# Performance work log

Hardware: AMD Instinct MI355X
Metric: run time of the kernel (lower is better)

The kernel has to match this reference:

```python
import jax, jax.numpy as jnp
import numpy as np
import math

B, C, HW = 4, 256, 32          # batch, seq_len (=channels), spatial side
D_MODEL = HW * HW              # 1024
OUT_C = 32 * 32                # 1024
D_STATE = 16
EXPAND = 2
D_INNER = EXPAND * D_MODEL     # 2048
DT_RANK = math.ceil(D_MODEL / 16)  # 64
D_CONV = 4


def setup_inputs() -> dict:
    key = jax.random.key(0)
    ks = jax.random.split(key, 12)
    s = 0.02
    x1 = jax.random.normal(ks[0], (B, C, HW, HW), dtype=jnp.float32)
    in_proj_w = jax.random.normal(ks[1], (2 * D_INNER, D_MODEL), dtype=jnp.float32) * s
    conv_w = jax.random.normal(ks[2], (D_INNER, 1, D_CONV), dtype=jnp.float32) * s
    conv_b = jnp.zeros((D_INNER,), dtype=jnp.float32)
    x_proj_w = jax.random.normal(ks[3], (DT_RANK + 2 * D_STATE, D_INNER), dtype=jnp.float32) * s
    dt_proj_w = jax.random.normal(ks[4], (D_INNER, DT_RANK), dtype=jnp.float32) * s
    dt_proj_b = jnp.zeros((D_INNER,), dtype=jnp.float32)
    A_log = jnp.log(jnp.broadcast_to(jnp.arange(1, D_STATE + 1, dtype=jnp.float32), (D_INNER, D_STATE)))
    D = jnp.ones((D_INNER,), dtype=jnp.float32)
    out_proj_w = jax.random.normal(ks[5], (OUT_C, D_INNER), dtype=jnp.float32) * s
    ln_w = jnp.ones((OUT_C,), dtype=jnp.float32)
    ln_b = jnp.zeros((OUT_C,), dtype=jnp.float32)
    return {"x1": x1, "in_proj_w": in_proj_w, "conv_w": conv_w, "conv_b": conv_b,
            "x_proj_w": x_proj_w, "dt_proj_w": dt_proj_w, "dt_proj_b": dt_proj_b,
            "A_log": A_log, "D": D, "out_proj_w": out_proj_w, "ln_w": ln_w, "ln_b": ln_b}


def _mamba_forward(x, in_proj_w, conv_w, conv_b, x_proj_w, dt_proj_w, dt_proj_b, A_log, D, out_proj_w):
    # x: (B, L, d_model)
    xz = jnp.einsum('bld,ed->ble', x, in_proj_w)            # (B,L,2*d_inner)
    xs, res = jnp.split(xz, 2, axis=-1)                     # each (B,L,d_inner)
    # depthwise causal conv1d, padding=d_conv-1 then truncate to L (== left pad)
    xs_c = jnp.transpose(xs, (0, 2, 1))                     # (B,d_inner,L)
    xs_c = jax.lax.conv_general_dilated(
        xs_c, conv_w, window_strides=(1,), padding=[(D_CONV - 1, 0)],
        dimension_numbers=('NCH', 'OIH', 'NCH'), feature_group_count=D_INNER)
    xs_c = xs_c + conv_b[None, :, None]
    xs = jax.nn.silu(jnp.transpose(xs_c, (0, 2, 1)))        # (B,L,d_inner)
    # input-dependent SSM parameters
    x_dbl = jnp.einsum('bld,ed->ble', xs, x_proj_w)         # (B,L,dt_rank+2N)
    dt, Bm, Cm = jnp.split(x_dbl, [DT_RANK, DT_RANK + D_STATE], axis=-1)
    delta = jax.nn.softplus(jnp.einsum('blr,dr->bld', dt, dt_proj_w) + dt_proj_b)  # (B,L,d_inner)
    A = -jnp.exp(A_log)                                     # (d_inner, N)
    deltaA = jnp.exp(delta[..., None] * A)                  # (B,L,d_inner,N)
    deltaB_u = delta[..., None] * Bm[:, :, None, :] * xs[..., None]  # (B,L,d_inner,N)

    def step(h, inp):
        dA, dBu, Ct = inp                                   # (B,d,N),(B,d,N),(B,N)
        h = dA * h + dBu
        y = jnp.einsum('bdn,bn->bd', h, Ct)
        return h, y

    h0 = jnp.zeros((deltaA.shape[0], D_INNER, D_STATE), dtype=deltaA.dtype)
    _, ys = jax.lax.scan(step, h0, (jnp.transpose(deltaA, (1, 0, 2, 3)),
                                    jnp.transpose(deltaB_u, (1, 0, 2, 3)),
                                    jnp.transpose(Cm, (1, 0, 2))))
    y = jnp.transpose(ys, (1, 0, 2))                        # (B,L,d_inner)
    y = y + D * xs
    y = y * jax.nn.silu(res)
    return jnp.einsum('bld,od->blo', y, out_proj_w)         # (B,L,out_c)


def reference(x1, in_proj_w, conv_w, conv_b, x_proj_w, dt_proj_w, dt_proj_b,
              A_log, D, out_proj_w, ln_w, ln_b):
    b, c, h, w = x1.shape
    x = x1.reshape(b, c, h * w)                             # (B, L=c, d_model)
    y = _mamba_forward(x, in_proj_w, conv_w, conv_b, x_proj_w, dt_proj_w,
                       dt_proj_b, A_log, D, out_proj_w)
    mu = jnp.mean(y, axis=-1, keepdims=True)
    var = jnp.var(y, axis=-1, keepdims=True)
    y = (y - mu) * jax.lax.rsqrt(var + 1e-5) * ln_w + ln_b
    return y.reshape(b, c, 32, 32)
```

## Files before the change

### kernel.cpp

```cpp
#include <hip/hip_runtime.h>
#include <hip/hip_bf16.h>
#include <math.h>

#define BATCH 4
#define SEQL 256
#define DMODEL 1024
#define DINNER 2048
#define DSTATE 16
#define DTRANK 64
#define OUTC 1024
#define NROWS (BATCH * SEQL)

typedef __attribute__((ext_vector_type(8))) short bf16x8;
typedef __attribute__((ext_vector_type(4))) float f32x4;

__global__ __launch_bounds__(256) void gemm_mfma(const __hip_bfloat16* __restrict__ A,
                                                 const __hip_bfloat16* __restrict__ B,
                                                 float* __restrict__ C,
                                                 int M, int N, int K,
                                                 int lda, int ldb) {
    __shared__ __hip_bfloat16 As[128 * 32];
    __shared__ __hip_bfloat16 Bs[128 * 32];
    const int t  = threadIdx.x;
    const int w  = t >> 6;
    const int ln = t & 63;
    const int wm = w >> 1, wn = w & 1;
    const int q  = ln >> 4, lr = ln & 15;
    const int m0 = blockIdx.y * 128;
    const int n0 = blockIdx.x * 128;
    const int Kpart = K / gridDim.z;
    const int kbase = blockIdx.z * Kpart;

    f32x4 acc[4][4] = {};

    const __hip_bfloat16* Ag = A + (size_t)m0 * lda + kbase;
    const __hip_bfloat16* Bg = B + (size_t)n0 * ldb + kbase;

    for (int k0 = 0; k0 < Kpart; k0 += 32) {
        #pragma unroll
        for (int i = 0; i < 2; ++i) {
            const int c = (i * 4 + w) * 64 + ln;
            const int r = c >> 2, col = (c & 3) * 8;
            __builtin_amdgcn_global_load_lds(
                (const __attribute__((address_space(1))) void*)(Ag + (size_t)r * lda + k0 + col),
                (__attribute__((address_space(3))) void*)(As + (i * 4 + w) * 64 * 8),
                16, 0, 0);
            __builtin_amdgcn_global_load_lds(
                (const __attribute__((address_space(1))) void*)(Bg + (size_t)r * ldb + k0 + col),
                (__attribute__((address_space(3))) void*)(Bs + (i * 4 + w) * 64 * 8),
                16, 0, 0);
        }
        __syncthreads();
        bf16x8 af[4], bfr[4];
        #pragma unroll
        for (int i = 0; i < 4; ++i)
            af[i] = *(const bf16x8*)(As + (wm * 64 + i * 16 + lr) * 32 + q * 8);
        #pragma unroll
        for (int j = 0; j < 4; ++j)
            bfr[j] = *(const bf16x8*)(Bs + (wn * 64 + j * 16 + lr) * 32 + q * 8);
        #pragma unroll
        for (int i = 0; i < 4; ++i)
            #pragma unroll
            for (int j = 0; j < 4; ++j)
                acc[i][j] = __builtin_amdgcn_mfma_f32_16x16x32_bf16(af[i], bfr[j], acc[i][j], 0, 0, 0);
        __syncthreads();
    }
    float* Cz = C + (size_t)blockIdx.z * M * N;
    #pragma unroll
    for (int i = 0; i < 4; ++i) {
        const int mrow = m0 + wm * 64 + i * 16 + q * 4;
        #pragma unroll
        for (int j = 0; j < 4; ++j) {
            const int ncol = n0 + wn * 64 + j * 16 + lr;
            #pragma unroll
            for (int r = 0; r < 4; ++r)
                Cz[(size_t)(mrow + r) * N + ncol] = acc[i][j][r];
        }
    }
}

__global__ __launch_bounds__(256) void gemm_dtsp(const __hip_bfloat16* __restrict__ A,
                                                 const __hip_bfloat16* __restrict__ B,
                                                 const float* __restrict__ bd,
                                                 float* __restrict__ delta) {
    __shared__ __hip_bfloat16 As[128 * 32];
    __shared__ __hip_bfloat16 Bs[128 * 32];
    const int t  = threadIdx.x;
    const int w  = t >> 6;
    const int ln = t & 63;
    const int wm = w >> 1, wn = w & 1;
    const int q  = ln >> 4, lr = ln & 15;
    const int m0 = blockIdx.y * 128;
    const int n0 = blockIdx.x * 128;
    const int lda = 128, ldb = 64, N = 2048;

    f32x4 acc[4][4] = {};
    const __hip_bfloat16* Ag = A + (size_t)m0 * lda;
    const __hip_bfloat16* Bg = B + (size_t)n0 * ldb;

    for (int k0 = 0; k0 < 64; k0 += 32) {
        #pragma unroll
        for (int i = 0; i < 2; ++i) {
            const int c = (i * 4 + w) * 64 + ln;
            const int r = c >> 2, col = (c & 3) * 8;
            __builtin_amdgcn_global_load_lds(
                (const __attribute__((address_space(1))) void*)(Ag + (size_t)r * lda + k0 + col),
                (__attribute__((address_space(3))) void*)(As + (i * 4 + w) * 64 * 8),
                16, 0, 0);
            __builtin_amdgcn_global_load_lds(
                (const __attribute__((address_space(1))) void*)(Bg + (size_t)r * ldb + k0 + col),
                (__attribute__((address_space(3))) void*)(Bs + (i * 4 + w) * 64 * 8),
                16, 0, 0);
        }
        __syncthreads();
        bf16x8 af[4], bfr[4];
        #pragma unroll
        for (int i = 0; i < 4; ++i)
            af[i] = *(const bf16x8*)(As + (wm * 64 + i * 16 + lr) * 32 + q * 8);
        #pragma unroll
        for (int j = 0; j < 4; ++j)
            bfr[j] = *(const bf16x8*)(Bs + (wn * 64 + j * 16 + lr) * 32 + q * 8);
        #pragma unroll
        for (int i = 0; i < 4; ++i)
            #pragma unroll
            for (int j = 0; j < 4; ++j)
                acc[i][j] = __builtin_amdgcn_mfma_f32_16x16x32_bf16(af[i], bfr[j], acc[i][j], 0, 0, 0);
        __syncthreads();
    }
    #pragma unroll
    for (int i = 0; i < 4; ++i) {
        const int mrow = m0 + wm * 64 + i * 16 + q * 4;
        #pragma unroll
        for (int j = 0; j < 4; ++j) {
            const int ncol = n0 + wn * 64 + j * 16 + lr;
            const float bias = bd[ncol];
            #pragma unroll
            for (int r = 0; r < 4; ++r) {
                float v = acc[i][j][r] + bias;
                float sp = (v > 20.f) ? v : log1pf(__expf(v));
                delta[(size_t)(mrow + r) * N + ncol] = sp;
            }
        }
    }
}

__global__ void xdbl_reduce_kernel(const float* __restrict__ part,
                                   float* __restrict__ xdbl,
                                   __hip_bfloat16* __restrict__ xdblb) {
    const int i = blockIdx.x * 256 + threadIdx.x;
    float s = 0.f;
    #pragma unroll
    for (int z = 0; z < 8; ++z) s += part[(size_t)z * (1024 * 128) + i];
    xdbl[i] = s;
    xdblb[i] = __float2bfloat16(s);
}

#define R0 (1024 * 1024)
#define R1 (R0 + 4096 * 1024)
#define R2 (R1 + 2048 * 1024)
#define R3 (R2 + 128 * 2048)
#define R4 (R3 + 2048 * 64)
__global__ void cast_all_kernel(const float* __restrict__ x1,
                                const float* __restrict__ w_in,
                                const float* __restrict__ w_out,
                                const float* __restrict__ w_xp,
                                const float* __restrict__ w_dt,
                                __hip_bfloat16* __restrict__ xa,
                                __hip_bfloat16* __restrict__ wb1,
                                __hip_bfloat16* __restrict__ wob,
                                __hip_bfloat16* __restrict__ wpb,
                                __hip_bfloat16* __restrict__ wdb) {
    int i = blockIdx.x * 256 + threadIdx.x;
    if (i < R0) {
        xa[i] = __float2bfloat16(x1[i]);
    } else if (i < R1) {
        int j = i - R0; wb1[j] = __float2bfloat16(w_in[j]);
    } else if (i < R2) {
        int j = i - R1; wob[j] = __float2bfloat16(w_out[j]);
    } else if (i < R3) {
        int j = i - R2; int e = j >> 11;
        wpb[j] = __float2bfloat16(e < 96 ? w_xp[j] : 0.f);
    } else if (i < R4) {
        int j = i - R3; wdb[j] = __float2bfloat16(w_dt[j]);
    }
}

__global__ void conv_silu_kernel(const float* __restrict__ xz,
                                 const float* __restrict__ conv_w,
                                 const float* __restrict__ conv_b,
                                 float* __restrict__ xs,
                                 __hip_bfloat16* __restrict__ xsb) {
    int idx = blockIdx.x * blockDim.x + threadIdx.x;
    int d = idx & (DINNER - 1);
    int l = (idx >> 11) & (SEQL - 1);
    int b = idx >> 19;
    const float w0 = conv_w[d * 4 + 0];
    const float w1 = conv_w[d * 4 + 1];
    const float w2 = conv_w[d * 4 + 2];
    const float w3 = conv_w[d * 4 + 3];
    float acc = conv_b[d];
    const size_t base = (size_t)(b * SEQL) * (2 * DINNER) + d;
    if (l >= 3) acc += w0 * xz[base + (size_t)(l - 3) * (2 * DINNER)];
    if (l >= 2) acc += w1 * xz[base + (size_t)(l - 2) * (2 * DINNER)];
    if (l >= 1) acc += w2 * xz[base + (size_t)(l - 1) * (2 * DINNER)];
    acc += w3 * xz[base + (size_t)l * (2 * DINNER)];
    float v = acc / (1.f + __expf(-acc));
    xs[idx] = v;
    xsb[idx] = __float2bfloat16(v);
}

__device__ __forceinline__ float row_reduce16(float x) {
    x += __int_as_float(__builtin_amdgcn_update_dpp(0, __float_as_int(x), 0x128, 0xF, 0xF, true));
    x += __int_as_float(__builtin_amdgcn_update_dpp(0, __float_as_int(x), 0x124, 0xF, 0xF, true));
    x += __int_as_float(__builtin_amdgcn_update_dpp(0, __float_as_int(x), 0x122, 0xF, 0xF, true));
    x += __int_as_float(__builtin_amdgcn_update_dpp(0, __float_as_int(x), 0x121, 0xF, 0xF, true));
    return x;
}

#define CHUNK 64
__global__ __launch_bounds__(256) void scan_kernel(const float* __restrict__ delta,
                                                   const float* __restrict__ xs,
                                                   const float* __restrict__ xdbl,
                                                   const float* __restrict__ xz,
                                                   const float* __restrict__ A_log,
                                                   const float* __restrict__ Dp,
                                                   __hip_bfloat16* __restrict__ ybb) {
    __shared__ float sDU[CHUNK][16][2];
    __shared__ float sBC[CHUNK][16][2];
    __shared__ float sGW[CHUNK][16][2];
    const int b = blockIdx.y;
    const int dg = blockIdx.x;
    const int t = threadIdx.x;
    const int dl = t >> 4;
    const int n  = t & 15;
    const int d  = dg * 16 + dl;
    const float a = -__expf(A_log[d * DSTATE + n]);
    const int srow = t >> 4, scol = t & 15;
    const int sd = dg * 16 + scol;
    const float Dstage = Dp[sd];
    const int rowbase = b * SEQL;
    float h = 0.f;

    float rD[4], rX[4], rR[4], rB[4], rC[4];

    auto issue_loads = [&](int l0) {
        #pragma unroll
        for (int i = 0; i < 4; ++i) {
            const int row = rowbase + l0 + i * 16 + srow;
            rD[i] = delta[(size_t)row * DINNER + sd];
            rX[i] = xs[(size_t)row * DINNER + sd];
            rR[i] = xz[(size_t)row * (2 * DINNER) + DINNER + sd];
            rB[i] = xdbl[row * 128 + 64 + scol];
            rC[i] = xdbl[row * 128 + 80 + scol];
        }
    };
    auto write_lds = [&]() {
        #pragma unroll
        for (int i = 0; i < 4; ++i) {
            const int row = i * 16 + srow;
            const float dv = rD[i], xv = rX[i], r = rR[i];
            const float g = r / (1.f + __expf(-r));
            sDU[row][scol][0] = dv;
            sDU[row][scol][1] = dv * xv;
            sGW[row][scol][0] = g;
            sGW[row][scol][1] = Dstage * xv * g;
            sBC[row][scol][0] = rB[i];
            sBC[row][scol][1] = rC[i];
        }
    };

    issue_loads(0);
    write_lds();
    __syncthreads();
    for (int c = 0; c < SEQL / CHUNK; ++c) {
        if (c + 1 < SEQL / CHUNK) issue_loads((c + 1) * CHUNK);
        const int l0 = c * CHUNK;
        #pragma unroll 16
        for (int l = 0; l < CHUNK; ++l) {
            const float dv = sDU[l][dl][0];
            const float u  = sDU[l][dl][1];
            const float bm = sBC[l][n][0];
            const float cm = sBC[l][n][1];
            const float e = __expf(dv * a);
            h = e * h + u * bm;
            float p = row_reduce16(h * cm);
            const float g  = sGW[l][dl][0];
            const float wg = sGW[l][dl][1];
            if (n == 0) {
                const float y = p * g + wg;
                ybb[(size_t)(rowbase + l0 + l) * DINNER + d] = __float2bfloat16(y);
            }
        }
        __syncthreads();
        if (c + 1 < SEQL / CHUNK) {
            write_lds();
        }
        __syncthreads();
    }
}

__global__ __launch_bounds__(256) void ln_kernel(const float* __restrict__ opart,
                                                 const float* __restrict__ lw,
                                                 const float* __restrict__ lb,
                                                 float* __restrict__ out) {
    __shared__ float red[8];
    const int row = blockIdx.x;
    const int t = threadIdx.x;
    float v[4];
    float s = 0.f, s2 = 0.f;
    #pragma unroll
    for (int i = 0; i < 4; ++i) {
        const int c = t + 256 * i;
        float acc = 0.f;
        #pragma unroll
        for (int z = 0; z < 4; ++z)
            acc += opart[(size_t)z * (1024 * 1024) + (size_t)row * OUTC + c];
        v[i] = acc;
        s += acc;
        s2 += acc * acc;
    }
    #pragma unroll
    for (int o = 32; o; o >>= 1) {
        s += __shfl_down(s, o);
        s2 += __shfl_down(s2, o);
    }
    const int wid = t >> 6;
    if ((t & 63) == 0) { red[wid] = s; red[4 + wid] = s2; }
    __syncthreads();
    if (t == 0) {
        float ts = red[0] + red[1] + red[2] + red[3];
        float ts2 = red[4] + red[5] + red[6] + red[7];
        float mu = ts * (1.f / OUTC);
        float var = ts2 * (1.f / OUTC) - mu * mu;
        red[0] = mu;
        red[1] = rsqrtf(var + 1e-5f);
    }
    __syncthreads();
    const float mu = red[0], rs = red[1];
    #pragma unroll
    for (int i = 0; i < 4; ++i) {
        const int c = t + 256 * i;
        out[(size_t)row * OUTC + c] = (v[i] - mu) * rs * lw[c] + lb[c];
    }
}

extern "C" void kernel_launch(void* const* d_in, const int* in_sizes, int n_in,
                              void* d_out, int out_size, void* d_ws, size_t ws_size,
                              hipStream_t stream) {
    const float* x1        = (const float*)d_in[0];
    const float* in_proj_w = (const float*)d_in[1];
    const float* conv_w    = (const float*)d_in[2];
    const float* conv_b    = (const float*)d_in[3];
    const float* x_proj_w  = (const float*)d_in[4];
    const float* dt_proj_w = (const float*)d_in[5];
    const float* dt_proj_b = (const float*)d_in[6];
    const float* A_log     = (const float*)d_in[7];
    const float* Dp        = (const float*)d_in[8];
    const float* out_proj_w= (const float*)d_in[9];
    const float* ln_w      = (const float*)d_in[10];
    const float* ln_b      = (const float*)d_in[11];
    float* out = (float*)d_out;

    char* p = (char*)d_ws;
    __hip_bfloat16* xa    = (__hip_bfloat16*)p; p += (size_t)1024 * 1024 * 2;
    __hip_bfloat16* wb1   = (__hip_bfloat16*)p; p += (size_t)4096 * 1024 * 2;
    __hip_bfloat16* wpb   = (__hip_bfloat16*)p; p += (size_t)128 * 2048 * 2;
    __hip_bfloat16* wob   = (__hip_bfloat16*)p; p += (size_t)1024 * 2048 * 2;
    __hip_bfloat16* wdb   = (__hip_bfloat16*)p; p += (size_t)2048 * 64 * 2;
    __hip_bfloat16* xsb   = (__hip_bfloat16*)p; p += (size_t)1024 * 2048 * 2;
    __hip_bfloat16* ybb   = (__hip_bfloat16*)p; p += (size_t)1024 * 2048 * 2;
    __hip_bfloat16* xdblb = (__hip_bfloat16*)p; p += (size_t)1024 * 128 * 2;
    float* xz    = (float*)p; p += (size_t)1024 * 4096 * 4;
    float* xs    = (float*)p; p += (size_t)1024 * 2048 * 4;
    float* xdbl  = (float*)p; p += (size_t)1024 * 128 * 4;
    float* xpart = (float*)p; p += (size_t)8 * 1024 * 128 * 4;
    float* delta = (float*)p; p += (size_t)1024 * 2048 * 4;
    float* opart = xz;

    cast_all_kernel<<<(R4 + 255) / 256, 256, 0, stream>>>(x1, in_proj_w, out_proj_w,
                                                          x_proj_w, dt_proj_w,
                                                          xa, wb1, wob, wpb, wdb);
    gemm_mfma<<<dim3(32, 8, 1), 256, 0, stream>>>(xa, wb1, xz,
                                                  NROWS, 2 * DINNER, DMODEL, DMODEL, DMODEL);
    conv_silu_kernel<<<(NROWS * DINNER) / 256, 256, 0, stream>>>(xz, conv_w, conv_b, xs, xsb);
    gemm_mfma<<<dim3(1, 8, 8), 256, 0, stream>>>(xsb, wpb, xpart,
                                                 NROWS, 128, DINNER, DINNER, DINNER);
    xdbl_reduce_kernel<<<(1024 * 128) / 256, 256, 0, stream>>>(xpart, xdbl, xdblb);
    gemm_dtsp<<<dim3(16, 8), 256, 0, stream>>>(xdblb, wdb, dt_proj_b, delta);
    scan_kernel<<<dim3(DINNER / 16, BATCH), 256, 0, stream>>>(delta, xs, xdbl, xz,
                                                              A_log, Dp, ybb);
    gemm_mfma<<<dim3(8, 8, 4), 256, 0, stream>>>(ybb, wob, opart,
                                                 NROWS, OUTC, DINNER, DINNER, DINNER);
    ln_kernel<<<NROWS, 256, 0, stream>>>(opart, ln_w, ln_b, out);
}
```

Baseline: 229.0 us.

## Split selective scan into chunk-carry and apply passes; double-buffer GEMM LDS tiles

The sequential 256-step scan is split into four 64-step chunks. A carry kernel computes each chunk's local end state and decay product. An apply kernel then combines the earlier chunks' carries and rescans its own chunk to produce outputs. This gives four times as many blocks and a quarter of the serial dependency chain, at the cost of reading delta, xs and B twice plus an extra launch and carry buffers. Separately, the MFMA GEMM now double-buffers its LDS tiles so the next K-tile's global-to-LDS loads overlap with the current tile's MFMAs.

Measured after the change: 221.1 us. 3.5% less time.

```diff
diff --git a/kernel.cpp b/kernel.cpp
--- a/kernel.cpp
+++ b/kernel.cpp
@@ -10,6 +10,8 @@
 #define DTRANK 64
 #define OUTC 1024
 #define NROWS (BATCH * SEQL)
+#define NCHUNK 4
+#define CH 64
 
 typedef __attribute__((ext_vector_type(8))) short bf16x8;
 typedef __attribute__((ext_vector_type(4))) float f32x4;
@@ -19,8 +21,8 @@
                                                  float* __restrict__ C,
                                                  int M, int N, int K,
                                                  int lda, int ldb) {
-    __shared__ __hip_bfloat16 As[128 * 32];
-    __shared__ __hip_bfloat16 Bs[128 * 32];
+    __shared__ __hip_bfloat16 As[2][128 * 32];
+    __shared__ __hip_bfloat16 Bs[2][128 * 32];
     const int t  = threadIdx.x;
     const int w  = t >> 6;
     const int ln = t & 63;
@@ -36,28 +38,35 @@
     const __hip_bfloat16* Ag = A + (size_t)m0 * lda + kbase;
     const __hip_bfloat16* Bg = B + (size_t)n0 * ldb + kbase;
 
-    for (int k0 = 0; k0 < Kpart; k0 += 32) {
+    auto stage = [&](int k0, int buf) {
         #pragma unroll
         for (int i = 0; i < 2; ++i) {
             const int c = (i * 4 + w) * 64 + ln;
             const int r = c >> 2, col = (c & 3) * 8;
             __builtin_amdgcn_global_load_lds(
                 (const __attribute__((address_space(1))) void*)(Ag + (size_t)r * lda + k0 + col),
-                (__attribute__((address_space(3))) void*)(As + (i * 4 + w) * 64 * 8),
+                (__attribute__((address_space(3))) void*)(As[buf] + (i * 4 + w) * 64 * 8),
                 16, 0, 0);
             __builtin_amdgcn_global_load_lds(
                 (const __attribute__((address_space(1))) void*)(Bg + (size_t)r * ldb + k0 + col),
-                (__attribute__((address_space(3))) void*)(Bs + (i * 4 + w) * 64 * 8),
+                (__attribute__((address_space(3))) void*)(Bs[buf] + (i * 4 + w) * 64 * 8),
                 16, 0, 0);
         }
-        __syncthreads();
+    };
+
+    const int nk = Kpart / 32;
+    stage(0, 0);
+    __syncthreads();
+    for (int kk = 0; kk < nk; ++kk) {
+        if (kk + 1 < nk) stage((kk + 1) * 32, (kk + 1) & 1);
+        const int buf = kk & 1;
         bf16x8 af[4], bfr[4];
         #pragma unroll
         for (int i = 0; i < 4; ++i)
-            af[i] = *(const bf16x8*)(As + (wm * 64 + i * 16 + lr) * 32 + q * 8);
+            af[i] = *(const bf16x8*)(As[buf] + (wm * 64 + i * 16 + lr) * 32 + q * 8);
         #pragma unroll
         for (int j = 0; j < 4; ++j)
-            bfr[j] = *(const bf16x8*)(Bs + (wn * 64 + j * 16 + lr) * 32 + q * 8);
+            bfr[j] = *(const bf16x8*)(Bs[buf] + (wn * 64 + j * 16 + lr) * 32 + q * 8);
         #pragma unroll
         for (int i = 0; i < 4; ++i)
             #pragma unroll
@@ -217,85 +226,95 @@
     return x;
 }
 
-#define CHUNK 64
-__global__ __launch_bounds__(256) void scan_kernel(const float* __restrict__ delta,
-                                                   const float* __restrict__ xs,
-                                                   const float* __restrict__ xdbl,
-                                                   const float* __restrict__ xz,
-                                                   const float* __restrict__ A_log,
-                                                   const float* __restrict__ Dp,
-                                                   __hip_bfloat16* __restrict__ ybb) {
-    __shared__ float sDU[CHUNK][16][2];
-    __shared__ float sBC[CHUNK][16][2];
-    __shared__ float sGW[CHUNK][16][2];
-    const int b = blockIdx.y;
-    const int dg = blockIdx.x;
+__global__ __launch_bounds__(256) void scan_carry_kernel(const float* __restrict__ delta,
+                                                         const float* __restrict__ xs,
+                                                         const float* __restrict__ xdbl,
+                                                         const float* __restrict__ A_log,
+                                                         float* __restrict__ carryL,
+                                                         float* __restrict__ carryP) {
+    __shared__ float sDU[CH][16][2];
+    __shared__ float sB[CH][16];
+    const int b = blockIdx.y, c = blockIdx.z, dg = blockIdx.x;
     const int t = threadIdx.x;
-    const int dl = t >> 4;
-    const int n  = t & 15;
-    const int d  = dg * 16 + dl;
+    const int dl = t >> 4, n = t & 15;
+    const int d = dg * 16 + dl;
+    const float a = -__expf(A_log[d * DSTATE + n]);
+    const int srow = t >> 4, scol = t & 15;
+    const int sd = dg * 16 + scol;
+    const int rowbase = b * SEQL + c * CH;
+    #pragma unroll
+    for (int i = 0; i < 4; ++i) {
+        const int row = rowbase + i * 16 + srow;
+        const float dv = delta[(size_t)row * DINNER + sd];
+        const float xv = xs[(size_t)row * DINNER + sd];
+        sDU[i * 16 + srow][scol][0] = dv;
+        sDU[i * 16 + srow][scol][1] = dv * xv;
+        sB[i * 16 + srow][scol] = xdbl[row * 128 + 64 + scol];
+    }
+    __syncthreads();
+    float h = 0.f, P = 1.f;
+    #pragma unroll 16
+    for (int l = 0; l < CH; ++l) {
+        const float e = __expf(sDU[l][dl][0] * a);
+        h = e * h + sDU[l][dl][1] * sB[l][n];
+        P *= e;
+    }
+    const size_t ci = (((size_t)(b * NCHUNK + c)) * DINNER + d) * DSTATE + n;
+    carryL[ci] = h;
+    carryP[ci] = P;
+}
+
+__global__ __launch_bounds__(256) void scan_apply_kernel(const float* __restrict__ delta,
+                                                         const float* __restrict__ xs,
+                                                         const float* __restrict__ xdbl,
+                                                         const float* __restrict__ xz,
+                                                         const float* __restrict__ A_log,
+                                                         const float* __restrict__ Dp,
+                                                         const float* __restrict__ carryL,
+                                                         const float* __restrict__ carryP,
+                                                         __hip_bfloat16* __restrict__ ybb) {
+    __shared__ float sDU[CH][16][2];
+    __shared__ float sBC[CH][16][2];
+    __shared__ float sGW[CH][16][2];
+    const int b = blockIdx.y, c = blockIdx.z, dg = blockIdx.x;
+    const int t = threadIdx.x;
+    const int dl = t >> 4, n = t & 15;
+    const int d = dg * 16 + dl;
     const float a = -__expf(A_log[d * DSTATE + n]);
     const int srow = t >> 4, scol = t & 15;
     const int sd = dg * 16 + scol;
     const float Dstage = Dp[sd];
-    const int rowbase = b * SEQL;
+    const int rowbase = b * SEQL + c * CH;
+    #pragma unroll
+    for (int i = 0; i < 4; ++i) {
+        const int row = rowbase + i * 16 + srow;
+        const float dv = delta[(size_t)row * DINNER + sd];
+        const float xv = xs[(size_t)row * DINNER + sd];
+        const float r  = xz[(size_t)row * (2 * DINNER) + DINNER + sd];
+        const float g = r / (1.f + __expf(-r));
+        const int lr_ = i * 16 + srow;
+        sDU[lr_][scol][0] = dv;
+        sDU[lr_][scol][1] = dv * xv;
+        sGW[lr_][scol][0] = g;
+        sGW[lr_][scol][1] = Dstage * xv * g;
+        sBC[lr_][scol][0] = xdbl[row * 128 + 64 + scol];
+        sBC[lr_][scol][1] = xdbl[row * 128 + 80 + scol];
+    }
+    __syncthreads();
     float h = 0.f;
-
-    float rD[4], rX[4], rR[4], rB[4], rC[4];
-
-    auto issue_loads = [&](int l0) {
-        #pragma unroll
-        for (int i = 0; i < 4; ++i) {
-            const int row = rowbase + l0 + i * 16 + srow;
-            rD[i] = delta[(size_t)row * DINNER + sd];
-            rX[i] = xs[(size_t)row * DINNER + sd];
-            rR[i] = xz[(size_t)row * (2 * DINNER) + DINNER + sd];
-            rB[i] = xdbl[row * 128 + 64 + scol];
-            rC[i] = xdbl[row * 128 + 80 + scol];
+    for (int j = 0; j < c; ++j) {
+        const size_t ci = (((size_t)(b * NCHUNK + j)) * DINNER + d) * DSTATE + n;
+        h = carryP[ci] * h + carryL[ci];
+    }
+    #pragma unroll 16
+    for (int l = 0; l < CH; ++l) {
+        const float e = __expf(sDU[l][dl][0] * a);
+        h = e * h + sDU[l][dl][1] * sBC[l][n][0];
+        float p = row_reduce16(h * sBC[l][n][1]);
+        if (n == 0) {
+            const float y = p * sGW[l][dl][0] + sGW[l][dl][1];
+            ybb[(size_t)(rowbase + l) * DINNER + d] = __float2bfloat16(y);
         }
-    };
-    auto write_lds = [&]() {
-        #pragma unroll
-        for (int i = 0; i < 4; ++i) {
-            const int row = i * 16 + srow;
-            const float dv = rD[i], xv = rX[i], r = rR[i];
-            const float g = r / (1.f + __expf(-r));
-            sDU[row][scol][0] = dv;
-            sDU[row][scol][1] = dv * xv;
-            sGW[row][scol][0] = g;
-            sGW[row][scol][1] = Dstage * xv * g;
-            sBC[row][scol][0] = rB[i];
-            sBC[row][scol][1] = rC[i];
-        }
-    };
-
-    issue_loads(0);
-    write_lds();
-    __syncthreads();
-    for (int c = 0; c < SEQL / CHUNK; ++c) {
-        if (c + 1 < SEQL / CHUNK) issue_loads((c + 1) * CHUNK);
-        const int l0 = c * CHUNK;
-        #pragma unroll 16
-        for (int l = 0; l < CHUNK; ++l) {
-            const float dv = sDU[l][dl][0];
-            const float u  = sDU[l][dl][1];
-            const float bm = sBC[l][n][0];
-            const float cm = sBC[l][n][1];
-            const float e = __expf(dv * a);
-            h = e * h + u * bm;
-            float p = row_reduce16(h * cm);
-            const float g  = sGW[l][dl][0];
-            const float wg = sGW[l][dl][1];
-            if (n == 0) {
-                const float y = p * g + wg;
-                ybb[(size_t)(rowbase + l0 + l) * DINNER + d] = __float2bfloat16(y);
-            }
-        }
-        __syncthreads();
-        if (c + 1 < SEQL / CHUNK) {
-            write_lds();
-        }
-        __syncthreads();
     }
 }
 
@@ -375,6 +394,8 @@
     float* xdbl  = (float*)p; p += (size_t)1024 * 128 * 4;
     float* xpart = (float*)p; p += (size_t)8 * 1024 * 128 * 4;
     float* delta = (float*)p; p += (size_t)1024 * 2048 * 4;
+    float* carryL = (float*)p; p += (size_t)BATCH * NCHUNK * DINNER * DSTATE * 4;
+    float* carryP = (float*)p; p += (size_t)BATCH * NCHUNK * DINNER * DSTATE * 4;
     float* opart = xz;
 
     cast_all_kernel<<<(R4 + 255) / 256, 256, 0, stream>>>(x1, in_proj_w, out_proj_w,
@@ -387,8 +408,10 @@
                                                  NROWS, 128, DINNER, DINNER, DINNER);
     xdbl_reduce_kernel<<<(1024 * 128) / 256, 256, 0, stream>>>(xpart, xdbl, xdblb);
     gemm_dtsp<<<dim3(16, 8), 256, 0, stream>>>(xdblb, wdb, dt_proj_b, delta);
-    scan_kernel<<<dim3(DINNER / 16, BATCH), 256, 0, stream>>>(delta, xs, xdbl, xz,
-                                                              A_log, Dp, ybb);
+    scan_carry_kernel<<<dim3(DINNER / 16, BATCH, NCHUNK), 256, 0, stream>>>(
+        delta, xs, xdbl, A_log, carryL, carryP);
+    scan_apply_kernel<<<dim3(DINNER / 16, BATCH, NCHUNK), 256, 0, stream>>>(
+        delta, xs, xdbl, xz, A_log, Dp, carryL, carryP, ybb);
     gemm_mfma<<<dim3(8, 8, 4), 256, 0, stream>>>(ybb, wob, opart,
                                                  NROWS, OUTC, DINNER, DINNER, DINNER);
     ln_kernel<<<NROWS, 256, 0, stream>>>(opart, ln_w, ln_b, out);
```
